# Optimization experiments

Hardware: AMD Instinct MI355X
Metric: run time of the kernel (lower is better)

Reference implementation:

```python
import jax, jax.numpy as jnp
import numpy as np

TEMPERATURE = 0.07
NEG = -1e9  # stand-in for -inf on the diagonal; exp(NEG) == 0


def setup_inputs() -> dict:
    key = jax.random.key(0)
    k1, k2, k3 = jax.random.split(key, 3)
    B, D = 4096, 1024
    return {
        "anchor_features": jax.random.normal(k1, (B, D), dtype=jnp.float32),
        "positive_features": jax.random.normal(k2, (B, D), dtype=jnp.float32),
        "labels": jax.random.randint(k3, (B,), 0, 2),
    }


def reference(anchor_features, positive_features, labels):
    B = anchor_features.shape[0]
    # L2-normalize (normalize=True)
    a = anchor_features / jnp.linalg.norm(anchor_features, axis=1, keepdims=True)
    p = positive_features / jnp.linalg.norm(positive_features, axis=1, keepdims=True)
    feats = jnp.concatenate([a, p], axis=0)                      # [2B, D]
    sim = jnp.matmul(feats, feats.T) / TEMPERATURE               # [2B, 2B]
    diag = jnp.eye(2 * B, dtype=bool)
    sim = jnp.where(diag, NEG, sim)                              # mask self-similarity
    # logsumexp over all non-self entries per row (diag contributes exp(NEG)=0)
    lse = jax.nn.logsumexp(sim, axis=1)                          # [2B]
    # positive pair similarity: sim[i, i+B] == sim[i+B, i] == <a_i, p_i>/t
    cross = jnp.sum(a * p, axis=1) / TEMPERATURE                 # [B]
    pos_sim = jnp.concatenate([cross, cross])                    # [2B]
    lab = jnp.concatenate([labels, labels]).astype(sim.dtype)    # [2B], 0/1
    per_row = (-pos_sim + lse) * lab
    num_pos = jnp.sum(lab)
    return jnp.where(num_pos > 0, jnp.sum(per_row) / num_pos, jnp.float32(0.0))
```

## Files before the change

kernel.cpp:

```cpp
#include <hip/hip_runtime.h>
#include <hip/hip_bf16.h>

#define TEMP_INV (1.0f / 0.07f)
#define LOG2E 1.4426950408889634f
#define LN2 0.6931471805599453f
#define CFIX 21.0f

typedef __attribute__((ext_vector_type(4))) float f32x4;
typedef __attribute__((ext_vector_type(8))) short bf16x8;

__device__ __forceinline__ ushort f2bf(float x) {
  union { float f; unsigned u; } v; v.f = x;
  unsigned r = (v.u + 0x7fffu + ((v.u >> 16) & 1u)) >> 16;
  return (ushort)r;
}

__device__ __forceinline__ void gload16(const ushort* g, ushort* l) {
  __builtin_amdgcn_global_load_lds(
      (const __attribute__((address_space(1))) void*)g,
      (__attribute__((address_space(3))) void*)l, 16, 0, 0);
}

__global__ __launch_bounds__(256) void zero_kernel(float* __restrict__ p, int n) {
  const int i = blockIdx.x * 256 + threadIdx.x;
  if (i < n) p[i] = 0.f;
}

__global__ __launch_bounds__(256) void norm_kernel(
    const float* __restrict__ A, const float* __restrict__ P,
    ushort* __restrict__ F, float* __restrict__ cross, int B, int D) {
  const int row = blockIdx.x;
  const int t = threadIdx.x;
  const float4* a4 = reinterpret_cast<const float4*>(A + (size_t)row * D);
  const float4* p4 = reinterpret_cast<const float4*>(P + (size_t)row * D);
  const int n4 = D >> 2;
  float sa = 0.f, sp = 0.f, sx = 0.f;
  for (int i = t; i < n4; i += 256) {
    float4 av = a4[i], pv = p4[i];
    sa += av.x * av.x + av.y * av.y + av.z * av.z + av.w * av.w;
    sp += pv.x * pv.x + pv.y * pv.y + pv.z * pv.z + pv.w * pv.w;
    sx += av.x * pv.x + av.y * pv.y + av.z * pv.z + av.w * pv.w;
  }
#pragma unroll
  for (int off = 32; off; off >>= 1) {
    sa += __shfl_down(sa, off);
    sp += __shfl_down(sp, off);
    sx += __shfl_down(sx, off);
  }
  __shared__ float red[3][4];
  const int wid = t >> 6, lane = t & 63;
  if (lane == 0) { red[0][wid] = sa; red[1][wid] = sp; red[2][wid] = sx; }
  __syncthreads();
  sa = red[0][0] + red[0][1] + red[0][2] + red[0][3];
  sp = red[1][0] + red[1][1] + red[1][2] + red[1][3];
  sx = red[2][0] + red[2][1] + red[2][2] + red[2][3];
  const float ia = rsqrtf(sa), ip = rsqrtf(sp);
  ushort* fa = F + (size_t)row * D;
  ushort* fp = F + (size_t)(B + row) * D;
  for (int i = t; i < n4; i += 256) {
    float4 av = a4[i], pv = p4[i];
    ushort4 oa, op;
    oa.x = f2bf(av.x * ia); oa.y = f2bf(av.y * ia);
    oa.z = f2bf(av.z * ia); oa.w = f2bf(av.w * ia);
    op.x = f2bf(pv.x * ip); op.y = f2bf(pv.y * ip);
    op.z = f2bf(pv.z * ip); op.w = f2bf(pv.w * ip);
    reinterpret_cast<ushort4*>(fa)[i] = oa;
    reinterpret_cast<ushort4*>(fp)[i] = op;
  }
  if (t == 0) cross[row] = sx * ia * ip;
}

#define VT 16

__global__ __launch_bounds__(512, 2) void gram_lse_kernel(
    const ushort* __restrict__ F, float* __restrict__ lsum, int NN, int D) {
  __shared__ ushort lds[2][2][2][8192];
  const int lin = blockIdx.x;
  int by = (int)((sqrtf(8.f * (float)lin + 1.f) - 1.f) * 0.5f);
  while ((by + 1) * (by + 2) / 2 <= lin) ++by;
  while (by * (by + 1) / 2 > lin) --by;
  const int bx = lin - by * (by + 1) / 2;
  const int r0 = bx * 256;
  const int c0 = by * 256;
  const bool offdiag = (bx != by);

  const int t = threadIdx.x;
  const int lane = t & 63, w = t >> 6;
  const int lo = lane & 15, hi = lane >> 4;
  const int wr = w >> 2, wn = w & 3;

  const int l3 = lane >> 3, l7 = lane & 7;
  const int cu = l7 ^ l3;
  const int sub = cu >> 2, kc = cu & 3;
  const int trow0 = w * 16 + l3 * 2 + sub;
  const int trow1 = (w + 8) * 16 + l3 * 2 + sub;
  const ushort* baseA0 = F + (size_t)(c0 + trow0) * D + kc * 8;
  const ushort* baseA1 = F + (size_t)(c0 + trow1) * D + kc * 8;
  const ushort* baseB0 = F + (size_t)(r0 + trow0) * D + kc * 8;
  const ushort* baseB1 = F + (size_t)(r0 + trow1) * D + kc * 8;
  const int dst0 = w * 512, dst1 = (w + 8) * 512;

  const int cA = (((lo & 1) << 2) | hi) ^ (lo >> 1);
  const int rdBase = (lo >> 1) * 128 + cA * 16;

#define STAGE_A(T, KS, BUF)                                              \
  do {                                                                   \
    int c_ = (T); if (c_ > VT - 1) c_ = VT - 1;                          \
    const size_t o_ = (size_t)(c_ * 64 + (KS) * 32);                     \
    gload16(baseA0 + o_, &lds[BUF][0][KS][dst0]);                        \
    gload16(baseA1 + o_, &lds[BUF][0][KS][dst1]);                        \
  } while (0)
#define STAGE_B(T, KS, BUF)                                              \
  do {                                                                   \
    int c_ = (T); if (c_ > VT - 1) c_ = VT - 1;                          \
    const size_t o_ = (size_t)(c_ * 64 + (KS) * 32);                     \
    gload16(baseB0 + o_, &lds[BUF][1][KS][dst0]);                        \
    gload16(baseB1 + o_, &lds[BUF][1][KS][dst1]);                        \
  } while (0)

  f32x4 acc[8][4];
  bf16x8 bfr[4];
  const float scl = LOG2E * TEMP_INV;

#define PHASE(BUF, MH, KS, READB, STAGE_STMT, WAIT4)                          \
  do {                                                                        \
    const char* RA_ = (const char*)&lds[BUF][0][KS][0];                       \
    const char* RB_ = (const char*)&lds[BUF][1][KS][0];                       \
    if (READB) {                                                              \
      _Pragma("unroll") for (int nf = 0; nf < 4; ++nf)                        \
          bfr[nf] = *(const bf16x8*)(RB_ + wn * 4096 + nf * 1024 + rdBase);   \
    }                                                                         \
    bf16x8 af[4];                                                             \
    _Pragma("unroll") for (int m = 0; m < 4; ++m)                             \
        af[m] = *(const bf16x8*)(RA_ + wr * 8192 + ((MH)*4 + m) * 1024 +      \
                                 rdBase);                                     \
    STAGE_STMT;                                                               \
    if (WAIT4) asm volatile("s_waitcnt vmcnt(4)" ::: "memory");               \
    asm volatile("" ::: "memory");                                            \
    __builtin_amdgcn_s_barrier();                                             \
    asm volatile("" ::: "memory");                                            \
    __builtin_amdgcn_s_setprio(1);                                            \
    _Pragma("unroll") for (int m = 0; m < 4; ++m)                             \
      _Pragma("unroll") for (int nf = 0; nf < 4; ++nf)                        \
          acc[(MH)*4 + m][nf] = __builtin_amdgcn_mfma_f32_16x16x32_bf16(      \
              af[m], bfr[nf], acc[(MH)*4 + m][nf], 0, 0, 0);                  \
    __builtin_amdgcn_s_setprio(0);                                            \
    asm volatile("" ::: "memory");                                            \
    __builtin_amdgcn_s_barrier();                                             \
    asm volatile("" ::: "memory");                                            \
  } while (0)

#pragma unroll
  for (int a = 0; a < 8; ++a)
#pragma unroll
    for (int b = 0; b < 4; ++b) acc[a][b] = (f32x4){0.f, 0.f, 0.f, 0.f};

  STAGE_A(0, 0, 0); STAGE_B(0, 0, 0);
  STAGE_A(0, 1, 0); STAGE_B(0, 1, 0);
  STAGE_A(1, 0, 1); STAGE_B(1, 0, 1);
  STAGE_B(1, 1, 1);
  asm volatile("s_waitcnt vmcnt(6)" ::: "memory");
  __builtin_amdgcn_s_barrier();
  asm volatile("" ::: "memory");

  for (int it = 0; it < 8; ++it) {
    const int tt = it * 2;
    PHASE(0, 0, 0, true,  STAGE_A(tt + 1, 1, 1), false);
    PHASE(0, 1, 0, false, STAGE_B(tt + 2, 0, 0), false);
    PHASE(0, 0, 1, true,  STAGE_A(tt + 2, 0, 0), false);
    PHASE(0, 1, 1, false, STAGE_B(tt + 2, 1, 0), true);
    PHASE(1, 0, 0, true,  STAGE_A(tt + 2, 1, 0), false);
    PHASE(1, 1, 0, false, STAGE_B(tt + 3, 0, 1), false);
    PHASE(1, 0, 1, true,  STAGE_A(tt + 3, 0, 1), false);
    PHASE(1, 1, 1, false, STAGE_B(tt + 3, 1, 1), true);
  }

  float s_i[4] = {0.f, 0.f, 0.f, 0.f};
  float s_j[32];
#pragma unroll
  for (int q = 0; q < 32; ++q) s_j[q] = 0.f;
  {
    const int jb2 = c0 + wr * 128;
#pragma unroll
    for (int nf = 0; nf < 4; ++nf) {
      const int dg = (r0 + wn * 64 + nf * 16 + lo) - jb2;
#pragma unroll
      for (int mf = 0; mf < 8; ++mf)
#pragma unroll
        for (int rg = 0; rg < 4; ++rg) {
          const int jloc = mf * 16 + hi * 4 + rg;
          const float e =
              (dg == jloc) ? 0.f : exp2f(acc[mf][nf][rg] * scl - CFIX);
          s_i[nf] += e;
          s_j[mf * 4 + rg] += e;
        }
    }
  }
#pragma unroll
  for (int nf = 0; nf < 4; ++nf) {
    float v = s_i[nf];
    v += __shfl_xor(v, 16);
    v += __shfl_xor(v, 32);
    if (hi == 0) atomicAdd(&lsum[r0 + wn * 64 + nf * 16 + lo], v);
  }
  if (offdiag) {
#pragma unroll
    for (int q = 0; q < 32; ++q) {
      float v = s_j[q];
      v += __shfl_xor(v, 1);
      v += __shfl_xor(v, 2);
      v += __shfl_xor(v, 4);
      v += __shfl_xor(v, 8);
      if (lo == 0)
        atomicAdd(&lsum[c0 + wr * 128 + (q >> 2) * 16 + hi * 4 + (q & 3)], v);
    }
  }

  asm volatile("s_waitcnt vmcnt(0)" ::: "memory");
#undef PHASE
#undef STAGE_A
#undef STAGE_B
}

__global__ __launch_bounds__(256) void finalize_part(
    const float* __restrict__ lsum, const float* __restrict__ cross,
    const int* __restrict__ labels, float* __restrict__ bsum,
    float* __restrict__ bcnt, int B) {
  const int NN = 2 * B;
  const int i = blockIdx.x * 256 + threadIdx.x;
  float sum = 0.f, cnt = 0.f;
  if (i < NN) {
    const float lse = LN2 * (CFIX + log2f(lsum[i]));
    const float lab = (float)labels[i % B];
    sum = (lse - cross[i % B] * TEMP_INV) * lab;
    cnt = lab;
  }
#pragma unroll
  for (int off = 32; off; off >>= 1) {
    sum += __shfl_down(sum, off);
    cnt += __shfl_down(cnt, off);
  }
  __shared__ float rs[4], rc[4];
  const int wid = threadIdx.x >> 6, lane = threadIdx.x & 63;
  if (lane == 0) { rs[wid] = sum; rc[wid] = cnt; }
  __syncthreads();
  if (threadIdx.x == 0) {
    bsum[blockIdx.x] = rs[0] + rs[1] + rs[2] + rs[3];
    bcnt[blockIdx.x] = rc[0] + rc[1] + rc[2] + rc[3];
  }
}

__global__ __launch_bounds__(64) void finalize_final(
    const float* __restrict__ bsum, const float* __restrict__ bcnt,
    float* __restrict__ out, int nb) {
  const int t = threadIdx.x;
  float s = (t < nb) ? bsum[t] : 0.f;
  float c = (t < nb) ? bcnt[t] : 0.f;
#pragma unroll
  for (int off = 32; off; off >>= 1) {
    s += __shfl_down(s, off);
    c += __shfl_down(c, off);
  }
  if (t == 0) out[0] = (c > 0.f) ? s / c : 0.f;
}

extern "C" void kernel_launch(void* const* d_in, const int* in_sizes, int n_in,
                              void* d_out, int out_size, void* d_ws, size_t ws_size,
                              hipStream_t stream) {
  const float* A = (const float*)d_in[0];
  const float* P = (const float*)d_in[1];
  const int* labels = (const int*)d_in[2];
  float* out = (float*)d_out;
  const int B = in_sizes[2];
  const int D = in_sizes[0] / B;
  const int NN = 2 * B;

  char* ws = (char*)d_ws;
  ushort* F = (ushort*)ws;
  size_t off = (size_t)NN * D * sizeof(ushort);
  off = (off + 255) & ~(size_t)255;
  float* cross = (float*)(ws + off);
  off += (size_t)B * sizeof(float);
  off = (off + 255) & ~(size_t)255;
  float* lsum = (float*)(ws + off);
  off += (size_t)NN * sizeof(float);
  off = (off + 255) & ~(size_t)255;
  float* bsum = (float*)(ws + off);
  off += 64 * sizeof(float);
  float* bcnt = (float*)(ws + off);

  zero_kernel<<<(NN + 255) / 256, 256, 0, stream>>>(lsum, NN);
  norm_kernel<<<B, 256, 0, stream>>>(A, P, F, cross, B, D);
  const int nrb = NN / 256;
  const int ntri = nrb * (nrb + 1) / 2;
  gram_lse_kernel<<<ntri, 512, 0, stream>>>(F, lsum, NN, D);
  const int nb = (NN + 255) / 256;
  finalize_part<<<nb, 256, 0, stream>>>(lsum, cross, labels, bsum, bcnt, B);
  finalize_final<<<1, 64, 0, stream>>>(bsum, bcnt, out, nb);
}
```

Before: 143.7 us.

## Shrink Gram tiles to 128x128 with 32x32 MFMA and XCD-aware block remap

Rewrites the symmetric Gram+LSE kernel to use 128x128 output tiles with 256-thread blocks, 32x32x16 bf16 MFMAs, a simple double-buffered K loop over 32-wide slices, and a block-index remap that groups consecutive triangle tiles per XCD. The aim is higher occupancy, more blocks to balance across CUs, and better L2 locality. In exchange each tile has lower arithmetic intensity, which doubles global/LDS traffic per FLOP, needs a barrier pair per 32-wide K step, and issues more atomics into lsum.

```diff
diff --git a/kernel.cpp b/kernel.cpp
--- a/kernel.cpp
+++ b/kernel.cpp
@@ -6,7 +6,7 @@
 #define LN2 0.6931471805599453f
 #define CFIX 21.0f
 
-typedef __attribute__((ext_vector_type(4))) float f32x4;
+typedef __attribute__((ext_vector_type(16))) float f32x16;
 typedef __attribute__((ext_vector_type(8))) short bf16x8;
 
 __device__ __forceinline__ ushort f2bf(float x) {
@@ -70,156 +70,166 @@
   if (t == 0) cross[row] = sx * ia * ip;
 }
 
-#define VT 16
-
-__global__ __launch_bounds__(512, 2) void gram_lse_kernel(
+__global__ __launch_bounds__(256, 4) void gram_lse_kernel(
     const ushort* __restrict__ F, float* __restrict__ lsum, int NN, int D) {
-  __shared__ ushort lds[2][2][2][8192];
-  const int lin = blockIdx.x;
+  __shared__ ushort lds[2][2][4096];
+  const int nrb = NN >> 7;
+  const int ntri = nrb * (nrb + 1) / 2;
+  int lin = blockIdx.x;
+  if ((ntri & 7) == 0) {
+    const int per = ntri >> 3;
+    lin = (lin & 7) * per + (lin >> 3);
+  }
   int by = (int)((sqrtf(8.f * (float)lin + 1.f) - 1.f) * 0.5f);
   while ((by + 1) * (by + 2) / 2 <= lin) ++by;
   while (by * (by + 1) / 2 > lin) --by;
   const int bx = lin - by * (by + 1) / 2;
-  const int r0 = bx * 256;
-  const int c0 = by * 256;
-  const bool offdiag = (bx != by);
+  const int r0 = bx * 128;
+  const int c0 = by * 128;
+  const bool diag = (bx == by);
 
   const int t = threadIdx.x;
   const int lane = t & 63, w = t >> 6;
-  const int lo = lane & 15, hi = lane >> 4;
-  const int wr = w >> 2, wn = w & 3;
+  const int l31 = lane & 31, l5 = lane >> 5;
+  const int wm = w >> 1, wn = w & 1;
 
   const int l3 = lane >> 3, l7 = lane & 7;
   const int cu = l7 ^ l3;
   const int sub = cu >> 2, kc = cu & 3;
-  const int trow0 = w * 16 + l3 * 2 + sub;
-  const int trow1 = (w + 8) * 16 + l3 * 2 + sub;
-  const ushort* baseA0 = F + (size_t)(c0 + trow0) * D + kc * 8;
-  const ushort* baseA1 = F + (size_t)(c0 + trow1) * D + kc * 8;
-  const ushort* baseB0 = F + (size_t)(r0 + trow0) * D + kc * 8;
-  const ushort* baseB1 = F + (size_t)(r0 + trow1) * D + kc * 8;
-  const int dst0 = w * 512, dst1 = (w + 8) * 512;
-
-  const int cA = (((lo & 1) << 2) | hi) ^ (lo >> 1);
-  const int rdBase = (lo >> 1) * 128 + cA * 16;
-
-#define STAGE_A(T, KS, BUF)                                              \
-  do {                                                                   \
-    int c_ = (T); if (c_ > VT - 1) c_ = VT - 1;                          \
-    const size_t o_ = (size_t)(c_ * 64 + (KS) * 32);                     \
-    gload16(baseA0 + o_, &lds[BUF][0][KS][dst0]);                        \
-    gload16(baseA1 + o_, &lds[BUF][0][KS][dst1]);                        \
+  const int trow0 = (w * 2 + 0) * 16 + l3 * 2 + sub;
+  const int trow1 = (w * 2 + 1) * 16 + l3 * 2 + sub;
+  const ushort* srcA0 = F + (size_t)(c0 + trow0) * D + kc * 8;
+  const ushort* srcA1 = F + (size_t)(c0 + trow1) * D + kc * 8;
+  const ushort* srcB0 = F + (size_t)(r0 + trow0) * D + kc * 8;
+  const ushort* srcB1 = F + (size_t)(r0 + trow1) * D + kc * 8;
+  const int dst0 = (w * 2 + 0) * 512;
+  const int dst1 = (w * 2 + 1) * 512;
+
+  int offA[2][2], offB[2][2];
+#pragma unroll
+  for (int m = 0; m < 2; ++m)
+#pragma unroll
+    for (int s = 0; s < 2; ++s) {
+      {
+        const int r = wm * 64 + m * 32 + l31;
+        const int lrow = r >> 1;
+        const int slot = ((r & 1) << 2) + (s << 1) + l5;
+        offA[m][s] = lrow * 128 + ((slot ^ (lrow & 7)) << 4);
+      }
+      {
+        const int r = wn * 64 + m * 32 + l31;
+        const int lrow = r >> 1;
+        const int slot = ((r & 1) << 2) + (s << 1) + l5;
+        offB[m][s] = lrow * 128 + ((slot ^ (lrow & 7)) << 4);
+      }
+    }
+
+  const int nv = D >> 5;
+
+#define STAGE(V, BUF)                                              \
+  do {                                                             \
+    int v_ = (V); if (v_ > nv - 1) v_ = nv - 1;                    \
+    const size_t o_ = (size_t)v_ * 32;                             \
+    gload16(srcA0 + o_, &lds[BUF][0][dst0]);                       \
+    gload16(srcA1 + o_, &lds[BUF][0][dst1]);                       \
+    gload16(srcB0 + o_, &lds[BUF][1][dst0]);                       \
+    gload16(srcB1 + o_, &lds[BUF][1][dst1]);                       \
   } while (0)
-#define STAGE_B(T, KS, BUF)                                              \
-  do {                                                                   \
-    int c_ = (T); if (c_ > VT - 1) c_ = VT - 1;                          \
-    const size_t o_ = (size_t)(c_ * 64 + (KS) * 32);                     \
-    gload16(baseB0 + o_, &lds[BUF][1][KS][dst0]);                        \
-    gload16(baseB1 + o_, &lds[BUF][1][KS][dst1]);                        \
-  } while (0)
-
-  f32x4 acc[8][4];
-  bf16x8 bfr[4];
+
+  f32x16 acc[2][2];
+#pragma unroll
+  for (int m = 0; m < 2; ++m)
+#pragma unroll
+    for (int n = 0; n < 2; ++n)
+#pragma unroll
+      for (int q = 0; q < 16; ++q) acc[m][n][q] = 0.f;
+
+  STAGE(0, 0);
+
+  for (int v = 0; v < nv; ++v) {
+    const int buf = v & 1;
+    STAGE(v + 1, buf ^ 1);
+    asm volatile("s_waitcnt vmcnt(4)" ::: "memory");
+    asm volatile("" ::: "memory");
+    __builtin_amdgcn_s_barrier();
+    asm volatile("" ::: "memory");
+
+    const char* RA = (const char*)&lds[buf][0][0];
+    const char* RB = (const char*)&lds[buf][1][0];
+    bf16x8 am[2][2], bn[2][2];
+#pragma unroll
+    for (int m = 0; m < 2; ++m)
+#pragma unroll
+      for (int s = 0; s < 2; ++s) {
+        am[m][s] = *(const bf16x8*)(RA + offA[m][s]);
+        bn[m][s] = *(const bf16x8*)(RB + offB[m][s]);
+      }
+
+    __builtin_amdgcn_s_setprio(1);
+#pragma unroll
+    for (int s = 0; s < 2; ++s)
+#pragma unroll
+      for (int m = 0; m < 2; ++m)
+#pragma unroll
+        for (int n = 0; n < 2; ++n)
+          acc[m][n] = __builtin_amdgcn_mfma_f32_32x32x16_bf16(
+              am[m][s], bn[n][s], acc[m][n], 0, 0, 0);
+    __builtin_amdgcn_s_setprio(0);
+
+    asm volatile("" ::: "memory");
+    __builtin_amdgcn_s_barrier();
+    asm volatile("" ::: "memory");
+  }
+
   const float scl = LOG2E * TEMP_INV;
-
-#define PHASE(BUF, MH, KS, READB, STAGE_STMT, WAIT4)                          \
-  do {                                                                        \
-    const char* RA_ = (const char*)&lds[BUF][0][KS][0];                       \
-    const char* RB_ = (const char*)&lds[BUF][1][KS][0];                       \
-    if (READB) {                                                              \
-      _Pragma("unroll") for (int nf = 0; nf < 4; ++nf)                        \
-          bfr[nf] = *(const bf16x8*)(RB_ + wn * 4096 + nf * 1024 + rdBase);   \
-    }                                                                         \
-    bf16x8 af[4];                                                             \
-    _Pragma("unroll") for (int m = 0; m < 4; ++m)                             \
-        af[m] = *(const bf16x8*)(RA_ + wr * 8192 + ((MH)*4 + m) * 1024 +      \
-                                 rdBase);                                     \
-    STAGE_STMT;                                                               \
-    if (WAIT4) asm volatile("s_waitcnt vmcnt(4)" ::: "memory");               \
-    asm volatile("" ::: "memory");                                            \
-    __builtin_amdgcn_s_barrier();                                             \
-    asm volatile("" ::: "memory");                                            \
-    __builtin_amdgcn_s_setprio(1);                                            \
-    _Pragma("unroll") for (int m = 0; m < 4; ++m)                             \
-      _Pragma("unroll") for (int nf = 0; nf < 4; ++nf)                        \
-          acc[(MH)*4 + m][nf] = __builtin_amdgcn_mfma_f32_16x16x32_bf16(      \
-              af[m], bfr[nf], acc[(MH)*4 + m][nf], 0, 0, 0);                  \
-    __builtin_amdgcn_s_setprio(0);                                            \
-    asm volatile("" ::: "memory");                                            \
-    __builtin_amdgcn_s_barrier();                                             \
-    asm volatile("" ::: "memory");                                            \
-  } while (0)
-
-#pragma unroll
-  for (int a = 0; a < 8; ++a)
-#pragma unroll
-    for (int b = 0; b < 4; ++b) acc[a][b] = (f32x4){0.f, 0.f, 0.f, 0.f};
-
-  STAGE_A(0, 0, 0); STAGE_B(0, 0, 0);
-  STAGE_A(0, 1, 0); STAGE_B(0, 1, 0);
-  STAGE_A(1, 0, 1); STAGE_B(1, 0, 1);
-  STAGE_B(1, 1, 1);
-  asm volatile("s_waitcnt vmcnt(6)" ::: "memory");
-  __builtin_amdgcn_s_barrier();
-  asm volatile("" ::: "memory");
-
-  for (int it = 0; it < 8; ++it) {
-    const int tt = it * 2;
-    PHASE(0, 0, 0, true,  STAGE_A(tt + 1, 1, 1), false);
-    PHASE(0, 1, 0, false, STAGE_B(tt + 2, 0, 0), false);
-    PHASE(0, 0, 1, true,  STAGE_A(tt + 2, 0, 0), false);
-    PHASE(0, 1, 1, false, STAGE_B(tt + 2, 1, 0), true);
-    PHASE(1, 0, 0, true,  STAGE_A(tt + 2, 1, 0), false);
-    PHASE(1, 1, 0, false, STAGE_B(tt + 3, 0, 1), false);
-    PHASE(1, 0, 1, true,  STAGE_A(tt + 3, 0, 1), false);
-    PHASE(1, 1, 1, false, STAGE_B(tt + 3, 1, 1), true);
-  }
-
-  float s_i[4] = {0.f, 0.f, 0.f, 0.f};
-  float s_j[32];
-#pragma unroll
-  for (int q = 0; q < 32; ++q) s_j[q] = 0.f;
-  {
-    const int jb2 = c0 + wr * 128;
-#pragma unroll
-    for (int nf = 0; nf < 4; ++nf) {
-      const int dg = (r0 + wn * 64 + nf * 16 + lo) - jb2;
-#pragma unroll
-      for (int mf = 0; mf < 8; ++mf)
-#pragma unroll
-        for (int rg = 0; rg < 4; ++rg) {
-          const int jloc = mf * 16 + hi * 4 + rg;
-          const float e =
-              (dg == jloc) ? 0.f : exp2f(acc[mf][nf][rg] * scl - CFIX);
-          s_i[nf] += e;
-          s_j[mf * 4 + rg] += e;
-        }
+  float s_i[2] = {0.f, 0.f};
+  float s_j[2][16];
+#pragma unroll
+  for (int m = 0; m < 2; ++m)
+#pragma unroll
+    for (int q = 0; q < 16; ++q) s_j[m][q] = 0.f;
+
+#pragma unroll
+  for (int m = 0; m < 2; ++m) {
+#pragma unroll
+    for (int n = 0; n < 2; ++n) {
+      const int il = wn * 64 + n * 32 + l31;
+#pragma unroll
+      for (int reg = 0; reg < 16; ++reg) {
+        const int jl = wm * 64 + m * 32 + (reg & 3) + ((reg >> 2) << 3) + (l5 << 2);
+        float e = exp2f(acc[m][n][reg] * scl - CFIX);
+        if (diag && il == jl) e = 0.f;
+        s_i[n] += e;
+        s_j[m][reg] += e;
+      }
     }
   }
 #pragma unroll
-  for (int nf = 0; nf < 4; ++nf) {
-    float v = s_i[nf];
-    v += __shfl_xor(v, 16);
+  for (int n = 0; n < 2; ++n) {
+    float v = s_i[n];
     v += __shfl_xor(v, 32);
-    if (hi == 0) atomicAdd(&lsum[r0 + wn * 64 + nf * 16 + lo], v);
-  }
-  if (offdiag) {
-#pragma unroll
-    for (int q = 0; q < 32; ++q) {
-      float v = s_j[q];
-      v += __shfl_xor(v, 1);
-      v += __shfl_xor(v, 2);
-      v += __shfl_xor(v, 4);
-      v += __shfl_xor(v, 8);
-      if (lo == 0)
-        atomicAdd(&lsum[c0 + wr * 128 + (q >> 2) * 16 + hi * 4 + (q & 3)], v);
-    }
+    if (l5 == 0) atomicAdd(&lsum[r0 + wn * 64 + n * 32 + l31], v);
+  }
+  if (!diag) {
+#pragma unroll
+    for (int m = 0; m < 2; ++m)
+#pragma unroll
+      for (int reg = 0; reg < 16; ++reg) {
+        float v = s_j[m][reg];
+        v += __shfl_xor(v, 1);
+        v += __shfl_xor(v, 2);
+        v += __shfl_xor(v, 4);
+        v += __shfl_xor(v, 8);
+        v += __shfl_xor(v, 16);
+        if (l31 == 0)
+          atomicAdd(&lsum[c0 + wm * 64 + m * 32 + (reg & 3) +
+                          ((reg >> 2) << 3) + (l5 << 2)],
+                    v);
+      }
   }
 
   asm volatile("s_waitcnt vmcnt(0)" ::: "memory");
-#undef PHASE
-#undef STAGE_A
-#undef STAGE_B
+#undef STAGE
 }
 
 __global__ __launch_bounds__(256) void finalize_part(
@@ -291,9 +301,9 @@
 
   zero_kernel<<<(NN + 255) / 256, 256, 0, stream>>>(lsum, NN);
   norm_kernel<<<B, 256, 0, stream>>>(A, P, F, cross, B, D);
-  const int nrb = NN / 256;
+  const int nrb = NN >> 7;
   const int ntri = nrb * (nrb + 1) / 2;
-  gram_lse_kernel<<<ntri, 512, 0, stream>>>(F, lsum, NN, D);
+  gram_lse_kernel<<<ntri, 256, 0, stream>>>(F, lsum, NN, D);
   const int nb = (NN + 255) / 256;
   finalize_part<<<nb, 256, 0, stream>>>(lsum, cross, labels, bsum, bcnt, B);
   finalize_final<<<1, 64, 0, stream>>>(bsum, bcnt, out, nb);
```

After: 154.3 us. +7.4%, slower.

## Make gram kernel persistent over triangular tiles and fold lsum zeroing into norm kernel

Applied to the files above, without the earlier changes.

The gram/logsumexp kernel now launches at most 256 persistent blocks, and each block walks a contiguous range of the triangular tile list instead of one block per tile. Diagonal masking is applied only on diagonal tiles. The separate zeroing kernel is removed, and norm_kernel clears lsum instead, which saves one launch. The goal is less block launch and scheduling overhead and better balance of the 528 tiles across the CUs. The cost is a serialised prologue per tile with an extra barrier, and a risk of tail imbalance because blocks get contiguous chunks.

```diff
diff --git a/kernel.cpp b/kernel.cpp
--- a/kernel.cpp
+++ b/kernel.cpp
@@ -21,16 +21,16 @@
       (__attribute__((address_space(3))) void*)l, 16, 0, 0);
 }
 
-__global__ __launch_bounds__(256) void zero_kernel(float* __restrict__ p, int n) {
-  const int i = blockIdx.x * 256 + threadIdx.x;
-  if (i < n) p[i] = 0.f;
-}
-
 __global__ __launch_bounds__(256) void norm_kernel(
     const float* __restrict__ A, const float* __restrict__ P,
-    ushort* __restrict__ F, float* __restrict__ cross, int B, int D) {
+    ushort* __restrict__ F, float* __restrict__ cross,
+    float* __restrict__ lsum, int B, int D) {
   const int row = blockIdx.x;
   const int t = threadIdx.x;
+  {
+    const int zi = row * 256 + t;
+    if (zi < 2 * B) lsum[zi] = 0.f;
+  }
   const float4* a4 = reinterpret_cast<const float4*>(A + (size_t)row * D);
   const float4* p4 = reinterpret_cast<const float4*>(P + (size_t)row * D);
   const int n4 = D >> 2;
@@ -75,14 +75,13 @@
 __global__ __launch_bounds__(512, 2) void gram_lse_kernel(
     const ushort* __restrict__ F, float* __restrict__ lsum, int NN, int D) {
   __shared__ ushort lds[2][2][2][8192];
-  const int lin = blockIdx.x;
-  int by = (int)((sqrtf(8.f * (float)lin + 1.f) - 1.f) * 0.5f);
-  while ((by + 1) * (by + 2) / 2 <= lin) ++by;
-  while (by * (by + 1) / 2 > lin) --by;
-  const int bx = lin - by * (by + 1) / 2;
-  const int r0 = bx * 256;
-  const int c0 = by * 256;
-  const bool offdiag = (bx != by);
+  const int nrb = NN >> 8;
+  const int ntri = nrb * (nrb + 1) / 2;
+  const int nblk = gridDim.x;
+  const int base = ntri / nblk, rem = ntri - base * nblk;
+  const int bid = blockIdx.x;
+  const int nMine = base + (bid < rem ? 1 : 0);
+  const int sMine = bid * base + (bid < rem ? bid : rem);
 
   const int t = threadIdx.x;
   const int lane = t & 63, w = t >> 6;
@@ -94,33 +93,45 @@
   const int sub = cu >> 2, kc = cu & 3;
   const int trow0 = w * 16 + l3 * 2 + sub;
   const int trow1 = (w + 8) * 16 + l3 * 2 + sub;
-  const ushort* baseA0 = F + (size_t)(c0 + trow0) * D + kc * 8;
-  const ushort* baseA1 = F + (size_t)(c0 + trow1) * D + kc * 8;
-  const ushort* baseB0 = F + (size_t)(r0 + trow0) * D + kc * 8;
-  const ushort* baseB1 = F + (size_t)(r0 + trow1) * D + kc * 8;
   const int dst0 = w * 512, dst1 = (w + 8) * 512;
 
   const int cA = (((lo & 1) << 2) | hi) ^ (lo >> 1);
   const int rdBase = (lo >> 1) * 128 + cA * 16;
+
+  const float scl = LOG2E * TEMP_INV;
+
+  for (int ti = 0; ti < nMine; ++ti) {
+    const int lin = sMine + ti;
+    int by = (int)((sqrtf(8.f * (float)lin + 1.f) - 1.f) * 0.5f);
+    while ((by + 1) * (by + 2) / 2 <= lin) ++by;
+    while (by * (by + 1) / 2 > lin) --by;
+    const int bx = lin - by * (by + 1) / 2;
+    const int r0 = bx * 256;
+    const int c0 = by * 256;
+    const bool diag = (bx == by);
+
+    const ushort* srcA0 = F + (size_t)(c0 + trow0) * D + kc * 8;
+    const ushort* srcA1 = F + (size_t)(c0 + trow1) * D + kc * 8;
+    const ushort* srcB0 = F + (size_t)(r0 + trow0) * D + kc * 8;
+    const ushort* srcB1 = F + (size_t)(r0 + trow1) * D + kc * 8;
 
 #define STAGE_A(T, KS, BUF)                                              \
   do {                                                                   \
     int c_ = (T); if (c_ > VT - 1) c_ = VT - 1;                          \
     const size_t o_ = (size_t)(c_ * 64 + (KS) * 32);                     \
-    gload16(baseA0 + o_, &lds[BUF][0][KS][dst0]);                        \
-    gload16(baseA1 + o_, &lds[BUF][0][KS][dst1]);                        \
+    gload16(srcA0 + o_, &lds[BUF][0][KS][dst0]);                         \
+    gload16(srcA1 + o_, &lds[BUF][0][KS][dst1]);                         \
   } while (0)
 #define STAGE_B(T, KS, BUF)                                              \
   do {                                                                   \
     int c_ = (T); if (c_ > VT - 1) c_ = VT - 1;                          \
     const size_t o_ = (size_t)(c_ * 64 + (KS) * 32);                     \
-    gload16(baseB0 + o_, &lds[BUF][1][KS][dst0]);                        \
-    gload16(baseB1 + o_, &lds[BUF][1][KS][dst1]);                        \
+    gload16(srcB0 + o_, &lds[BUF][1][KS][dst0]);                         \
+    gload16(srcB1 + o_, &lds[BUF][1][KS][dst1]);                         \
   } while (0)
 
-  f32x4 acc[8][4];
-  bf16x8 bfr[4];
-  const float scl = LOG2E * TEMP_INV;
+    f32x4 acc[8][4];
+    bf16x8 bfr[4];
 
 #define PHASE(BUF, MH, KS, READB, STAGE_STMT, WAIT4)                          \
   do {                                                                        \
@@ -151,75 +162,78 @@
   } while (0)
 
 #pragma unroll
-  for (int a = 0; a < 8; ++a)
-#pragma unroll
-    for (int b = 0; b < 4; ++b) acc[a][b] = (f32x4){0.f, 0.f, 0.f, 0.f};
-
-  STAGE_A(0, 0, 0); STAGE_B(0, 0, 0);
-  STAGE_A(0, 1, 0); STAGE_B(0, 1, 0);
-  STAGE_A(1, 0, 1); STAGE_B(1, 0, 1);
-  STAGE_B(1, 1, 1);
-  asm volatile("s_waitcnt vmcnt(6)" ::: "memory");
-  __builtin_amdgcn_s_barrier();
-  asm volatile("" ::: "memory");
-
-  for (int it = 0; it < 8; ++it) {
-    const int tt = it * 2;
-    PHASE(0, 0, 0, true,  STAGE_A(tt + 1, 1, 1), false);
-    PHASE(0, 1, 0, false, STAGE_B(tt + 2, 0, 0), false);
-    PHASE(0, 0, 1, true,  STAGE_A(tt + 2, 0, 0), false);
-    PHASE(0, 1, 1, false, STAGE_B(tt + 2, 1, 0), true);
-    PHASE(1, 0, 0, true,  STAGE_A(tt + 2, 1, 0), false);
-    PHASE(1, 1, 0, false, STAGE_B(tt + 3, 0, 1), false);
-    PHASE(1, 0, 1, true,  STAGE_A(tt + 3, 0, 1), false);
-    PHASE(1, 1, 1, false, STAGE_B(tt + 3, 1, 1), true);
-  }
-
-  float s_i[4] = {0.f, 0.f, 0.f, 0.f};
-  float s_j[32];
-#pragma unroll
-  for (int q = 0; q < 32; ++q) s_j[q] = 0.f;
-  {
-    const int jb2 = c0 + wr * 128;
+    for (int a = 0; a < 8; ++a)
+#pragma unroll
+      for (int b = 0; b < 4; ++b) acc[a][b] = (f32x4){0.f, 0.f, 0.f, 0.f};
+
+    STAGE_A(0, 0, 0); STAGE_B(0, 0, 0);
+    STAGE_A(0, 1, 0); STAGE_B(0, 1, 0);
+    STAGE_A(1, 0, 1); STAGE_B(1, 0, 1);
+    STAGE_B(1, 1, 1);
+    asm volatile("s_waitcnt vmcnt(6)" ::: "memory");
+    __builtin_amdgcn_s_barrier();
+    asm volatile("" ::: "memory");
+
+    for (int it = 0; it < 8; ++it) {
+      const int tt = it * 2;
+      PHASE(0, 0, 0, true,  STAGE_A(tt + 1, 1, 1), false);
+      PHASE(0, 1, 0, false, STAGE_B(tt + 2, 0, 0), false);
+      PHASE(0, 0, 1, true,  STAGE_A(tt + 2, 0, 0), false);
+      PHASE(0, 1, 1, false, STAGE_B(tt + 2, 1, 0), true);
+      PHASE(1, 0, 0, true,  STAGE_A(tt + 2, 1, 0), false);
+      PHASE(1, 1, 0, false, STAGE_B(tt + 3, 0, 1), false);
+      PHASE(1, 0, 1, true,  STAGE_A(tt + 3, 0, 1), false);
+      PHASE(1, 1, 1, false, STAGE_B(tt + 3, 1, 1), true);
+    }
+
+    float s_i[4] = {0.f, 0.f, 0.f, 0.f};
+    float s_j[32];
+#pragma unroll
+    for (int q = 0; q < 32; ++q) s_j[q] = 0.f;
+    {
+      const int jb2 = c0 + wr * 128;
+#pragma unroll
+      for (int nf = 0; nf < 4; ++nf) {
+        const int dg = (r0 + wn * 64 + nf * 16 + lo) - jb2;
+#pragma unroll
+        for (int mf = 0; mf < 8; ++mf)
+#pragma unroll
+          for (int rg = 0; rg < 4; ++rg) {
+            const int jloc = mf * 16 + hi * 4 + rg;
+            float e = exp2f(acc[mf][nf][rg] * scl - CFIX);
+            if (diag && dg == jloc) e = 0.f;
+            s_i[nf] += e;
+            s_j[mf * 4 + rg] += e;
+          }
+      }
+    }
 #pragma unroll
     for (int nf = 0; nf < 4; ++nf) {
-      const int dg = (r0 + wn * 64 + nf * 16 + lo) - jb2;
-#pragma unroll
-      for (int mf = 0; mf < 8; ++mf)
-#pragma unroll
-        for (int rg = 0; rg < 4; ++rg) {
-          const int jloc = mf * 16 + hi * 4 + rg;
-          const float e =
-              (dg == jloc) ? 0.f : exp2f(acc[mf][nf][rg] * scl - CFIX);
-          s_i[nf] += e;
-          s_j[mf * 4 + rg] += e;
-        }
+      float v = s_i[nf];
+      v += __shfl_xor(v, 16);
+      v += __shfl_xor(v, 32);
+      if (hi == 0) atomicAdd(&lsum[r0 + wn * 64 + nf * 16 + lo], v);
     }
-  }
-#pragma unroll
-  for (int nf = 0; nf < 4; ++nf) {
-    float v = s_i[nf];
-    v += __shfl_xor(v, 16);
-    v += __shfl_xor(v, 32);
-    if (hi == 0) atomicAdd(&lsum[r0 + wn * 64 + nf * 16 + lo], v);
-  }
-  if (offdiag) {
-#pragma unroll
-    for (int q = 0; q < 32; ++q) {
-      float v = s_j[q];
-      v += __shfl_xor(v, 1);
-      v += __shfl_xor(v, 2);
-      v += __shfl_xor(v, 4);
-      v += __shfl_xor(v, 8);
-      if (lo == 0)
-        atomicAdd(&lsum[c0 + wr * 128 + (q >> 2) * 16 + hi * 4 + (q & 3)], v);
+    if (!diag) {
+#pragma unroll
+      for (int q = 0; q < 32; ++q) {
+        float v = s_j[q];
+        v += __shfl_xor(v, 1);
+        v += __shfl_xor(v, 2);
+        v += __shfl_xor(v, 4);
+        v += __shfl_xor(v, 8);
+        if (lo == 0)
+          atomicAdd(&lsum[c0 + wr * 128 + (q >> 2) * 16 + hi * 4 + (q & 3)], v);
+      }
     }
-  }
-
-  asm volatile("s_waitcnt vmcnt(0)" ::: "memory");
+
+    asm volatile("s_waitcnt vmcnt(0)" ::: "memory");
+    __builtin_amdgcn_s_barrier();
+    asm volatile("" ::: "memory");
 #undef PHASE
 #undef STAGE_A
 #undef STAGE_B
+  }
 }
 
 __global__ __launch_bounds__(256) void finalize_part(
@@ -289,11 +303,11 @@
   off += 64 * sizeof(float);
   float* bcnt = (float*)(ws + off);
 
-  zero_kernel<<<(NN + 255) / 256, 256, 0, stream>>>(lsum, NN);
-  norm_kernel<<<B, 256, 0, stream>>>(A, P, F, cross, B, D);
-  const int nrb = NN / 256;
+  norm_kernel<<<B, 256, 0, stream>>>(A, P, F, cross, lsum, B, D);
+  const int nrb = NN >> 8;
   const int ntri = nrb * (nrb + 1) / 2;
-  gram_lse_kernel<<<ntri, 512, 0, stream>>>(F, lsum, NN, D);
+  const int nblk = (ntri < 256) ? ntri : 256;
+  gram_lse_kernel<<<nblk, 512, 0, stream>>>(F, lsum, NN, D);
   const int nb = (NN + 255) / 256;
   finalize_part<<<nb, 256, 0, stream>>>(lsum, cross, labels, bsum, bcnt, B);
   finalize_final<<<1, 64, 0, stream>>>(bsum, bcnt, out, nb);
```

Result: faster. 128.8 us (-10.3%).
